# Kernel tuning notes

Hardware: AMD Instinct MI355X
Metric: run time of the kernel (lower is better)

## Reference

```python
import jax, jax.numpy as jnp
import numpy as np

TANH_CONST = 2.5
TEMPERATURE = 5.0


def setup_inputs() -> dict:
    key = jax.random.key(0)
    ks = jax.random.split(key, 9)
    B, L, NB, H, NC = 16384, 64, 8, 128, 1000
    return {
        "class_ids": jax.random.randint(ks[0], (B,), 0, NC),
        "gumbel_u": jax.random.uniform(ks[1], (L, B, NB), dtype=jnp.float32),
        "g_emb": jax.random.normal(ks[2], (NC, H), dtype=jnp.float32) * 0.1,
        "w_emb": jax.random.normal(ks[3], (NB, H), dtype=jnp.float32) * 0.1,
        "w_soft": jax.random.normal(ks[4], (NB, H), dtype=jnp.float32) * 0.1,
        "w_ih": jax.random.normal(ks[5], (4 * H, H), dtype=jnp.float32) * 0.1,
        "w_hh": jax.random.normal(ks[6], (4 * H, H), dtype=jnp.float32) * 0.1,
        "b_ih": jax.random.normal(ks[7], (4 * H,), dtype=jnp.float32) * 0.1,
        "b_hh": jax.random.normal(ks[8], (4 * H,), dtype=jnp.float32) * 0.1,
    }


def reference(class_ids, gumbel_u, g_emb, w_emb, w_soft, w_ih, w_hh, b_ih, b_hh):
    B = class_ids.shape[0]
    H = g_emb.shape[1]
    x0 = g_emb[class_ids]                      # [B, H] class embedding (reused each step)
    h0 = jnp.zeros((B, H), x0.dtype)
    c0 = jnp.zeros((B, H), x0.dtype)

    def step(carry, u):
        h, c, x = carry
        gates = x @ w_ih.T + h @ w_hh.T + b_ih + b_hh   # [B, 4H], torch gate order i,f,g,o
        i, f, g, o = jnp.split(gates, 4, axis=-1)
        c2 = jax.nn.sigmoid(f) * c + jax.nn.sigmoid(i) * jnp.tanh(g)
        h2 = jax.nn.sigmoid(o) * jnp.tanh(c2)
        logit = h2 @ w_soft.T                           # [B, NB]
        logit = TANH_CONST * jnp.tanh(logit / TEMPERATURE)
        # categorical sample via gumbel-max
        uc = jnp.clip(u, 1e-8, 1.0 - 1e-8)
        gmb = -jnp.log(-jnp.log(uc))
        branch = jnp.argmax(logit + gmb, axis=-1)       # [B] int
        logp = jax.nn.log_softmax(logit, axis=-1)
        lp = jnp.take_along_axis(logp, branch[:, None], axis=1)[:, 0]
        ent = -jnp.sum(jnp.exp(logp) * logp, axis=-1)
        x2 = (w_emb[branch] + x0) * 0.5
        return (h2, c2, x2), (branch, lp, ent)

    _, (arcs, lps, ents) = jax.lax.scan(step, (h0, c0, x0), gumbel_u)
    # stack along dim=1 like torch.stack(..., dim=1) -> [B, L]
    sample_arc = arcs.T
    sample_log_prob = lps.T
    sample_entropy = ents.T
    sample_prob = jnp.exp(sample_log_prob)
    return sample_arc, sample_log_prob, sample_entropy, sample_prob
```

## Files before the change

kernel.cpp:

```cpp
#include <hip/hip_runtime.h>
#include <math.h>

#define HD 128
#define NBR 8
#define LSTEPS 64
#define TILE_B 32
#define HT_PAD 36
#define PART_PAD 132

#define WPT_OFF   0
#define WIPT_OFF  65536
#define PP_OFF    131072
#define BSUM_OFF  135168

__global__ __launch_bounds__(256) void setup_kernel(
    const float* __restrict__ w_emb, const float* __restrict__ w_ih,
    const float* __restrict__ w_hh, const float* __restrict__ b_ih,
    const float* __restrict__ b_hh, float* __restrict__ ws)
{
  int tid = blockIdx.x * blockDim.x + threadIdx.x;
  if (tid < 65536) {
    int k = tid >> 9, col = tid & 511;
    int hh = col >> 2, q = col & 3;
    ws[WPT_OFF + tid]  = w_hh[(q*HD + hh)*HD + k];
    ws[WIPT_OFF + tid] = w_ih[(q*HD + hh)*HD + k];
  }
  if (tid < 4096) {
    int j = tid >> 9, rem = tid & 511;
    int q = rem >> 7, hh2 = rem & 127;
    const float* wr = w_ih + (q*HD + hh2)*HD;
    const float* er = w_emb + j*HD;
    float s = 0.f;
    for (int k = 0; k < HD; ++k) s = fmaf(er[k], wr[k], s);
    ws[PP_OFF + (size_t)j*512 + 4*hh2 + q] = s + b_ih[q*HD + hh2] + b_hh[q*HD + hh2];
  }
  if (tid < 512) {
    int q = tid >> 7, hh2 = tid & 127;
    ws[BSUM_OFF + tid] = b_ih[q*HD + hh2] + b_hh[q*HD + hh2];
  }
}

__device__ __forceinline__ float fsig(float x) {
  return __fdividef(1.f, 1.f + __expf(-x));
}
__device__ __forceinline__ float ftanh(float x) {
  float ax = fabsf(x);
  float e  = __expf(-2.f * ax);
  float r  = __fdividef(1.f - e, 1.f + e);
  return copysignf(r, x);
}

#define ROWQ(qi, wq, HA, HB) \
  acc[qi][0] = fmaf((HA).x, wq, acc[qi][0]); acc[qi][1] = fmaf((HA).y, wq, acc[qi][1]); \
  acc[qi][2] = fmaf((HA).z, wq, acc[qi][2]); acc[qi][3] = fmaf((HA).w, wq, acc[qi][3]); \
  acc[qi][4] = fmaf((HB).x, wq, acc[qi][4]); acc[qi][5] = fmaf((HB).y, wq, acc[qi][5]); \
  acc[qi][6] = fmaf((HB).z, wq, acc[qi][6]); acc[qi][7] = fmaf((HB).w, wq, acc[qi][7]);

#define KFMA(W, HA, HB) \
  ROWQ(0, (W).x, HA, HB) ROWQ(1, (W).y, HA, HB) ROWQ(2, (W).z, HA, HB) ROWQ(3, (W).w, HA, HB)

#define BAR_LGKM() asm volatile("s_waitcnt lgkmcnt(0)\n\ts_barrier" ::: "memory")

__global__ __launch_bounds__(512, 4) void ctrl_kernel(
    const int* __restrict__ class_ids,
    const float* __restrict__ gumbel_u,
    const float* __restrict__ g_emb,
    const float* __restrict__ w_soft,
    const float* __restrict__ ws,
    float* __restrict__ out,
    int Btot)
{
  __shared__ __align__(16) float hT0[HD * HT_PAD];
  __shared__ __align__(16) float hT1[HD * HT_PAD];
  __shared__ __align__(16) float wsoft_l[NBR * HD];
  __shared__ __align__(16) float part_l[TILE_B * PART_PAD];
  __shared__ __align__(16) float pp_l[NBR * 512];
  __shared__ int br_l[TILE_B];

  const int tid = threadIdx.x;
  const int b0  = blockIdx.x * TILE_B;
  const size_t BL = (size_t)Btot * LSTEPS;

  const float* __restrict__ wpT  = ws + WPT_OFF;
  const float* __restrict__ wipT = ws + WIPT_OFF;

  for (int i = tid; i < NBR*HD; i += 512) wsoft_l[i] = w_soft[i];
  for (int i = tid; i < NBR*512; i += 512) pp_l[i] = ws[PP_OFF + i];

  const int hh = tid & 127;
  const int bg = tid >> 7;
  const int slb = tid >> 4;
  const int sr  = tid & 15;

  {
    int sb = tid >> 4;
    int kc = tid & 15;
    int cid = class_ids[b0 + sb];
    const float* src = g_emb + (size_t)cid * HD + kc*8;
    float4 v0 = *(const float4*)(src);
    float4 v1 = *(const float4*)(src + 4);
    int kb = kc*8;
    hT0[(kb+0)*HT_PAD + sb] = v0.x;
    hT0[(kb+1)*HT_PAD + sb] = v0.y;
    hT0[(kb+2)*HT_PAD + sb] = v0.z;
    hT0[(kb+3)*HT_PAD + sb] = v0.w;
    hT0[(kb+4)*HT_PAD + sb] = v1.x;
    hT0[(kb+5)*HT_PAD + sb] = v1.y;
    hT0[(kb+6)*HT_PAD + sb] = v1.z;
    hT0[(kb+7)*HT_PAD + sb] = v1.w;
  }
  __syncthreads();

  float qpark[32];
  {
    float acc[4][8];
    #pragma unroll
    for (int q = 0; q < 4; ++q)
      #pragma unroll
      for (int j = 0; j < 8; ++j) acc[q][j] = 0.f;

    const float* wr = wipT + 4*hh;
    const float* hr = hT0 + bg*8;
    #pragma unroll 2
    for (int k = 0; k < HD; ++k) {
      float4 w  = *(const float4*)(wr);
      float4 ha = *(const float4*)(hr);
      float4 hb = *(const float4*)(hr + 4);
      KFMA(w, ha, hb);
      wr += 512; hr += HT_PAD;
    }
    #pragma unroll
    for (int q = 0; q < 4; ++q) {
      float bs = ws[BSUM_OFF + q*HD + hh];
      #pragma unroll
      for (int j = 0; j < 8; ++j) {
        float v = 0.5f * (acc[q][j] + bs);
        asm("v_accvgpr_write_b32 %0, %1" : "=a"(qpark[q*8+j]) : "v"(v));
      }
    }
  }
  __syncthreads();

  float c[8];
  #pragma unroll
  for (int j = 0; j < 8; ++j) c[j] = 0.f;

  float* hcur = hT0;
  float* hnxt = hT1;

  for (int t = 0; t < LSTEPS; ++t) {
    float gmb[8];
    if (sr == 0) {
      const float* up = gumbel_u + ((size_t)t * Btot + (b0 + slb)) * NBR;
      float4 ua = *(const float4*)up;
      float4 ub = *(const float4*)(up + 4);
      float uv[8] = {ua.x,ua.y,ua.z,ua.w,ub.x,ub.y,ub.z,ub.w};
      #pragma unroll
      for (int nb = 0; nb < 8; ++nb) {
        float uc = fminf(fmaxf(uv[nb], 1e-8f), 0.99999999f);
        gmb[nb] = -__logf(-__logf(uc));
      }
    }

    float acc[4][8];
    #pragma unroll
    for (int q = 0; q < 4; ++q)
      #pragma unroll
      for (int j = 0; j < 8; ++j)
        asm("v_accvgpr_read_b32 %0, %1" : "=v"(acc[q][j]) : "a"(qpark[q*8+j]));

    if (t > 0) {
      __builtin_amdgcn_s_setprio(1);
      const float* wr = wpT + 4*hh;
      const float* hr = hcur + bg*8;
      float4 w0 = *(const float4*)(wr);
      float4 w1 = *(const float4*)(wr + 512);
      float4 a0 = *(const float4*)(hr);
      float4 b0v = *(const float4*)(hr + 4);
      float4 a1 = *(const float4*)(hr + HT_PAD);
      float4 b1 = *(const float4*)(hr + HT_PAD + 4);
      #pragma unroll 3
      for (int kb = 0; kb < 63; ++kb) {
        float4 wc = w0, ac = a0, bc = b0v;
        w0  = *(const float4*)(wr + 2*512);
        a0  = *(const float4*)(hr + 2*HT_PAD);
        b0v = *(const float4*)(hr + 2*HT_PAD + 4);
        KFMA(wc, ac, bc);
        float4 wd = w1, ad = a1, bd = b1;
        w1 = *(const float4*)(wr + 3*512);
        a1 = *(const float4*)(hr + 3*HT_PAD);
        b1 = *(const float4*)(hr + 3*HT_PAD + 4);
        KFMA(wd, ad, bd);
        wr += 1024; hr += 2*HT_PAD;
      }
      KFMA(w0, a0, b0v);
      KFMA(w1, a1, b1);
      __builtin_amdgcn_s_setprio(0);
    }

    float h2v[8];
    #pragma unroll
    for (int j = 0; j < 8; ++j) {
      float gi, gf, gg, go;
      if (t == 0) {
        gi = 2.f*acc[0][j]; gf = 2.f*acc[1][j];
        gg = 2.f*acc[2][j]; go = 2.f*acc[3][j];
      } else {
        int br = br_l[bg*8 + j];
        float4 pv = *(const float4*)(&pp_l[br*512 + 4*hh]);
        gi = fmaf(0.5f, pv.x, acc[0][j]);
        gf = fmaf(0.5f, pv.y, acc[1][j]);
        gg = fmaf(0.5f, pv.z, acc[2][j]);
        go = fmaf(0.5f, pv.w, acc[3][j]);
      }
      float iv = fsig(gi);
      float fv = fsig(gf);
      float gv = ftanh(gg);
      float ov = fsig(go);
      float c2 = fmaf(fv, c[j], iv*gv);
      c[j] = c2;
      h2v[j] = ov * ftanh(c2);
    }

    {
      float* dst = &hnxt[hh*HT_PAD + bg*8];
      *(float4*)(dst)   = make_float4(h2v[0],h2v[1],h2v[2],h2v[3]);
      *(float4*)(dst+4) = make_float4(h2v[4],h2v[5],h2v[6],h2v[7]);
    }
    BAR_LGKM();

    {
      int lb = tid & 31, ch = tid >> 5;
      const float* hp = hnxt + (ch*8)*HT_PAD + lb;
      float hv[8];
      #pragma unroll
      for (int i = 0; i < 8; ++i) hv[i] = hp[i*HT_PAD];
      #pragma unroll
      for (int nb = 0; nb < 8; ++nb) {
        const float4* wr2 = (const float4*)&wsoft_l[nb*HD + ch*8];
        float4 wa = wr2[0], wb = wr2[1];
        float p = 0.f;
        p = fmaf(hv[0], wa.x, p); p = fmaf(hv[1], wa.y, p);
        p = fmaf(hv[2], wa.z, p); p = fmaf(hv[3], wa.w, p);
        p = fmaf(hv[4], wb.x, p); p = fmaf(hv[5], wb.y, p);
        p = fmaf(hv[6], wb.z, p); p = fmaf(hv[7], wb.w, p);
        part_l[lb*PART_PAD + nb*16 + ch] = p;
      }
    }
    BAR_LGKM();

    {
      float s[8];
      #pragma unroll
      for (int nb = 0; nb < 8; ++nb)
        s[nb] = part_l[slb*PART_PAD + nb*16 + sr];
      #pragma unroll
      for (int mk = 1; mk < 16; mk <<= 1) {
        #pragma unroll
        for (int nb = 0; nb < 8; ++nb)
          s[nb] += __shfl_xor(s[nb], mk, 64);
      }
      if (sr == 0) {
        float lg[8];
        #pragma unroll
        for (int nb = 0; nb < 8; ++nb)
          lg[nb] = 2.5f * ftanh(s[nb] * 0.2f);
        int br = 0; float best = lg[0] + gmb[0];
        #pragma unroll
        for (int nb = 1; nb < 8; ++nb) {
          float y = lg[nb] + gmb[nb];
          if (y > best) { best = y; br = nb; }
        }
        br_l[slb] = br;
        float m = lg[0];
        #pragma unroll
        for (int nb = 1; nb < 8; ++nb) m = fmaxf(m, lg[nb]);
        float se = 0.f;
        #pragma unroll
        for (int nb = 0; nb < 8; ++nb) se += __expf(lg[nb] - m);
        float lse = __logf(se);
        float lp = (lg[br] - m) - lse;
        float ent = 0.f;
        #pragma unroll
        for (int nb = 0; nb < 8; ++nb) {
          float lpi = (lg[nb] - m) - lse;
          ent -= __expf(lpi) * lpi;
        }
        size_t row = (size_t)(b0 + slb) * LSTEPS + t;
        out[row]        = (float)br;
        out[BL + row]   = lp;
        out[2*BL + row] = ent;
        out[3*BL + row] = __expf(lp);
      }
    }
    BAR_LGKM();

    float* tmp = hcur; hcur = hnxt; hnxt = tmp;
  }
}

extern "C" void kernel_launch(void* const* d_in, const int* in_sizes, int n_in,
                              void* d_out, int out_size, void* d_ws, size_t ws_size,
                              hipStream_t stream) {
  const int*   class_ids = (const int*)d_in[0];
  const float* gumbel_u  = (const float*)d_in[1];
  const float* g_emb     = (const float*)d_in[2];
  const float* w_emb     = (const float*)d_in[3];
  const float* w_soft    = (const float*)d_in[4];
  const float* w_ih      = (const float*)d_in[5];
  const float* w_hh      = (const float*)d_in[6];
  const float* b_ih      = (const float*)d_in[7];
  const float* b_hh      = (const float*)d_in[8];
  float* out = (float*)d_out;
  float* ws  = (float*)d_ws;
  int B = in_sizes[0];

  hipLaunchKernelGGL(setup_kernel, dim3(256), dim3(256), 0, stream,
                     w_emb, w_ih, w_hh, b_ih, b_hh, ws);
  hipLaunchKernelGGL(ctrl_kernel, dim3(B / TILE_B), dim3(512), 0, stream,
                     class_ids, gumbel_u, g_emb, w_soft, ws, out, B);
}
```

Baseline: 2.282 ms.

## Halve block threads and give each thread 16 batch columns per gate

Drops the recurrent LSTM kernel from 512 to 256 threads per block, so each thread now computes 4 gates × 16 batch rows instead of 4 × 8. Each loaded weight float4 is reused across twice as many batch rows, which cuts global/L2 weight traffic per FMA, and the logit reduction and scratch padding are resized to match. The cost is twice the register pressure for accumulators and parked AGPR values, and launch bounds drop to 256 threads × 2 blocks. That lowers occupancy and latency hiding, and the per-step serial work per thread doubles.

```diff
diff --git a/kernel.cpp b/kernel.cpp
--- a/kernel.cpp
+++ b/kernel.cpp
@@ -6,7 +6,7 @@
 #define LSTEPS 64
 #define TILE_B 32
 #define HT_PAD 36
-#define PART_PAD 132
+#define PART_PAD 68
 
 #define WPT_OFF   0
 #define WIPT_OFF  65536
@@ -50,18 +50,28 @@
   return copysignf(r, x);
 }
 
-#define ROWQ(qi, wq, HA, HB) \
-  acc[qi][0] = fmaf((HA).x, wq, acc[qi][0]); acc[qi][1] = fmaf((HA).y, wq, acc[qi][1]); \
-  acc[qi][2] = fmaf((HA).z, wq, acc[qi][2]); acc[qi][3] = fmaf((HA).w, wq, acc[qi][3]); \
-  acc[qi][4] = fmaf((HB).x, wq, acc[qi][4]); acc[qi][5] = fmaf((HB).y, wq, acc[qi][5]); \
-  acc[qi][6] = fmaf((HB).z, wq, acc[qi][6]); acc[qi][7] = fmaf((HB).w, wq, acc[qi][7]);
-
-#define KFMA(W, HA, HB) \
-  ROWQ(0, (W).x, HA, HB) ROWQ(1, (W).y, HA, HB) ROWQ(2, (W).z, HA, HB) ROWQ(3, (W).w, HA, HB)
+#define ROWQ16(qi, wq) \
+  acc[qi][0]  = fmaf(ha.x, wq, acc[qi][0]);  acc[qi][1]  = fmaf(ha.y, wq, acc[qi][1]);  \
+  acc[qi][2]  = fmaf(ha.z, wq, acc[qi][2]);  acc[qi][3]  = fmaf(ha.w, wq, acc[qi][3]);  \
+  acc[qi][4]  = fmaf(hb.x, wq, acc[qi][4]);  acc[qi][5]  = fmaf(hb.y, wq, acc[qi][5]);  \
+  acc[qi][6]  = fmaf(hb.z, wq, acc[qi][6]);  acc[qi][7]  = fmaf(hb.w, wq, acc[qi][7]);  \
+  acc[qi][8]  = fmaf(hc.x, wq, acc[qi][8]);  acc[qi][9]  = fmaf(hc.y, wq, acc[qi][9]);  \
+  acc[qi][10] = fmaf(hc.z, wq, acc[qi][10]); acc[qi][11] = fmaf(hc.w, wq, acc[qi][11]); \
+  acc[qi][12] = fmaf(hd.x, wq, acc[qi][12]); acc[qi][13] = fmaf(hd.y, wq, acc[qi][13]); \
+  acc[qi][14] = fmaf(hd.z, wq, acc[qi][14]); acc[qi][15] = fmaf(hd.w, wq, acc[qi][15]);
+
+#define KFMA16(W) \
+  ROWQ16(0, (W).x) ROWQ16(1, (W).y) ROWQ16(2, (W).z) ROWQ16(3, (W).w)
+
+#define LOADH(HP) \
+  float4 ha = *(const float4*)(HP); \
+  float4 hb = *(const float4*)((HP) + 4); \
+  float4 hc = *(const float4*)((HP) + 8); \
+  float4 hd = *(const float4*)((HP) + 12);
 
 #define BAR_LGKM() asm volatile("s_waitcnt lgkmcnt(0)\n\ts_barrier" ::: "memory")
 
-__global__ __launch_bounds__(512, 4) void ctrl_kernel(
+__global__ __launch_bounds__(256, 2) void ctrl_kernel(
     const int* __restrict__ class_ids,
     const float* __restrict__ gumbel_u,
     const float* __restrict__ g_emb,
@@ -84,66 +94,63 @@
   const float* __restrict__ wpT  = ws + WPT_OFF;
   const float* __restrict__ wipT = ws + WIPT_OFF;
 
-  for (int i = tid; i < NBR*HD; i += 512) wsoft_l[i] = w_soft[i];
-  for (int i = tid; i < NBR*512; i += 512) pp_l[i] = ws[PP_OFF + i];
+  for (int i = tid; i < NBR*HD; i += 256) wsoft_l[i] = w_soft[i];
+  for (int i = tid; i < NBR*512; i += 256) pp_l[i] = ws[PP_OFF + i];
 
   const int hh = tid & 127;
   const int bg = tid >> 7;
-  const int slb = tid >> 4;
-  const int sr  = tid & 15;
+  const int slb = tid >> 3;
+  const int sr  = tid & 7;
 
   {
-    int sb = tid >> 4;
-    int kc = tid & 15;
+    int sb = tid >> 3;
+    int kc = tid & 7;
     int cid = class_ids[b0 + sb];
-    const float* src = g_emb + (size_t)cid * HD + kc*8;
-    float4 v0 = *(const float4*)(src);
-    float4 v1 = *(const float4*)(src + 4);
-    int kb = kc*8;
-    hT0[(kb+0)*HT_PAD + sb] = v0.x;
-    hT0[(kb+1)*HT_PAD + sb] = v0.y;
-    hT0[(kb+2)*HT_PAD + sb] = v0.z;
-    hT0[(kb+3)*HT_PAD + sb] = v0.w;
-    hT0[(kb+4)*HT_PAD + sb] = v1.x;
-    hT0[(kb+5)*HT_PAD + sb] = v1.y;
-    hT0[(kb+6)*HT_PAD + sb] = v1.z;
-    hT0[(kb+7)*HT_PAD + sb] = v1.w;
+    const float* src = g_emb + (size_t)cid * HD + kc*16;
+    #pragma unroll
+    for (int ii = 0; ii < 4; ++ii) {
+      float4 v = *(const float4*)(src + 4*ii);
+      int kb = kc*16 + 4*ii;
+      hT0[(kb+0)*HT_PAD + sb] = v.x;
+      hT0[(kb+1)*HT_PAD + sb] = v.y;
+      hT0[(kb+2)*HT_PAD + sb] = v.z;
+      hT0[(kb+3)*HT_PAD + sb] = v.w;
+    }
   }
   __syncthreads();
 
-  float qpark[32];
+  float qpark[64];
   {
-    float acc[4][8];
+    float acc[4][16];
     #pragma unroll
     for (int q = 0; q < 4; ++q)
       #pragma unroll
-      for (int j = 0; j < 8; ++j) acc[q][j] = 0.f;
+      for (int j = 0; j < 16; ++j) acc[q][j] = 0.f;
 
     const float* wr = wipT + 4*hh;
-    const float* hr = hT0 + bg*8;
+    const float* hr = hT0 + bg*16;
     #pragma unroll 2
     for (int k = 0; k < HD; ++k) {
-      float4 w  = *(const float4*)(wr);
-      float4 ha = *(const float4*)(hr);
-      float4 hb = *(const float4*)(hr + 4);
-      KFMA(w, ha, hb);
+      float4 w = *(const float4*)(wr);
+      LOADH(hr);
+      KFMA16(w);
       wr += 512; hr += HT_PAD;
     }
     #pragma unroll
     for (int q = 0; q < 4; ++q) {
       float bs = ws[BSUM_OFF + q*HD + hh];
       #pragma unroll
-      for (int j = 0; j < 8; ++j) {
+      for (int j = 0; j < 16; ++j) {
         float v = 0.5f * (acc[q][j] + bs);
-        asm("v_accvgpr_write_b32 %0, %1" : "=a"(qpark[q*8+j]) : "v"(v));
+        asm("v_accvgpr_write_b32 %0, %1" : "=a"(qpark[q*16+j]) : "v"(v));
       }
     }
   }
   __syncthreads();
 
-  float c[8];
+  float c[16];
   #pragma unroll
-  for (int j = 0; j < 8; ++j) c[j] = 0.f;
+  for (int j = 0; j < 16; ++j) c[j] = 0.f;
 
   float* hcur = hT0;
   float* hnxt = hT1;
@@ -162,51 +169,49 @@
       }
     }
 
-    float acc[4][8];
+    float acc[4][16];
     #pragma unroll
     for (int q = 0; q < 4; ++q)
       #pragma unroll
-      for (int j = 0; j < 8; ++j)
-        asm("v_accvgpr_read_b32 %0, %1" : "=v"(acc[q][j]) : "a"(qpark[q*8+j]));
+      for (int j = 0; j < 16; ++j)
+        asm("v_accvgpr_read_b32 %0, %1" : "=v"(acc[q][j]) : "a"(qpark[q*16+j]));
 
     if (t > 0) {
       __builtin_amdgcn_s_setprio(1);
       const float* wr = wpT + 4*hh;
-      const float* hr = hcur + bg*8;
+      const float* hr = hcur + bg*16;
       float4 w0 = *(const float4*)(wr);
       float4 w1 = *(const float4*)(wr + 512);
-      float4 a0 = *(const float4*)(hr);
-      float4 b0v = *(const float4*)(hr + 4);
-      float4 a1 = *(const float4*)(hr + HT_PAD);
-      float4 b1 = *(const float4*)(hr + HT_PAD + 4);
-      #pragma unroll 3
+      #pragma unroll 2
       for (int kb = 0; kb < 63; ++kb) {
-        float4 wc = w0, ac = a0, bc = b0v;
-        w0  = *(const float4*)(wr + 2*512);
-        a0  = *(const float4*)(hr + 2*HT_PAD);
-        b0v = *(const float4*)(hr + 2*HT_PAD + 4);
-        KFMA(wc, ac, bc);
-        float4 wd = w1, ad = a1, bd = b1;
-        w1 = *(const float4*)(wr + 3*512);
-        a1 = *(const float4*)(hr + 3*HT_PAD);
-        b1 = *(const float4*)(hr + 3*HT_PAD + 4);
-        KFMA(wd, ad, bd);
+        {
+          float4 wc = w0;
+          w0 = *(const float4*)(wr + 2*512);
+          LOADH(hr);
+          KFMA16(wc);
+        }
+        {
+          float4 wc = w1;
+          w1 = *(const float4*)(wr + 3*512);
+          LOADH(hr + HT_PAD);
+          KFMA16(wc);
+        }
         wr += 1024; hr += 2*HT_PAD;
       }
-      KFMA(w0, a0, b0v);
-      KFMA(w1, a1, b1);
+      { LOADH(hr);          KFMA16(w0); }
+      { LOADH(hr + HT_PAD); KFMA16(w1); }
       __builtin_amdgcn_s_setprio(0);
     }
 
-    float h2v[8];
-    #pragma unroll
-    for (int j = 0; j < 8; ++j) {
+    float h2v[16];
+    #pragma unroll
+    for (int j = 0; j < 16; ++j) {
       float gi, gf, gg, go;
       if (t == 0) {
         gi = 2.f*acc[0][j]; gf = 2.f*acc[1][j];
         gg = 2.f*acc[2][j]; go = 2.f*acc[3][j];
       } else {
-        int br = br_l[bg*8 + j];
+        int br = br_l[bg*16 + j];
         float4 pv = *(const float4*)(&pp_l[br*512 + 4*hh]);
         gi = fmaf(0.5f, pv.x, acc[0][j]);
         gf = fmaf(0.5f, pv.y, acc[1][j]);
@@ -223,28 +228,34 @@
     }
 
     {
-      float* dst = &hnxt[hh*HT_PAD + bg*8];
-      *(float4*)(dst)   = make_float4(h2v[0],h2v[1],h2v[2],h2v[3]);
-      *(float4*)(dst+4) = make_float4(h2v[4],h2v[5],h2v[6],h2v[7]);
+      float* dst = &hnxt[hh*HT_PAD + bg*16];
+      *(float4*)(dst)    = make_float4(h2v[0], h2v[1], h2v[2], h2v[3]);
+      *(float4*)(dst+4)  = make_float4(h2v[4], h2v[5], h2v[6], h2v[7]);
+      *(float4*)(dst+8)  = make_float4(h2v[8], h2v[9], h2v[10],h2v[11]);
+      *(float4*)(dst+12) = make_float4(h2v[12],h2v[13],h2v[14],h2v[15]);
     }
     BAR_LGKM();
 
     {
       int lb = tid & 31, ch = tid >> 5;
-      const float* hp = hnxt + (ch*8)*HT_PAD + lb;
-      float hv[8];
-      #pragma unroll
-      for (int i = 0; i < 8; ++i) hv[i] = hp[i*HT_PAD];
+      const float* hp = hnxt + (ch*16)*HT_PAD + lb;
+      float hv[16];
+      #pragma unroll
+      for (int i = 0; i < 16; ++i) hv[i] = hp[i*HT_PAD];
       #pragma unroll
       for (int nb = 0; nb < 8; ++nb) {
-        const float4* wr2 = (const float4*)&wsoft_l[nb*HD + ch*8];
-        float4 wa = wr2[0], wb = wr2[1];
+        const float4* wr2 = (const float4*)&wsoft_l[nb*HD + ch*16];
+        float4 wa = wr2[0], wb = wr2[1], wc = wr2[2], wd = wr2[3];
         float p = 0.f;
-        p = fmaf(hv[0], wa.x, p); p = fmaf(hv[1], wa.y, p);
-        p = fmaf(hv[2], wa.z, p); p = fmaf(hv[3], wa.w, p);
-        p = fmaf(hv[4], wb.x, p); p = fmaf(hv[5], wb.y, p);
-        p = fmaf(hv[6], wb.z, p); p = fmaf(hv[7], wb.w, p);
-        part_l[lb*PART_PAD + nb*16 + ch] = p;
+        p = fmaf(hv[0],  wa.x, p); p = fmaf(hv[1],  wa.y, p);
+        p = fmaf(hv[2],  wa.z, p); p = fmaf(hv[3],  wa.w, p);
+        p = fmaf(hv[4],  wb.x, p); p = fmaf(hv[5],  wb.y, p);
+        p = fmaf(hv[6],  wb.z, p); p = fmaf(hv[7],  wb.w, p);
+        p = fmaf(hv[8],  wc.x, p); p = fmaf(hv[9],  wc.y, p);
+        p = fmaf(hv[10], wc.z, p); p = fmaf(hv[11], wc.w, p);
+        p = fmaf(hv[12], wd.x, p); p = fmaf(hv[13], wd.y, p);
+        p = fmaf(hv[14], wd.z, p); p = fmaf(hv[15], wd.w, p);
+        part_l[lb*PART_PAD + nb*8 + ch] = p;
       }
     }
     BAR_LGKM();
@@ -253,9 +264,9 @@
       float s[8];
       #pragma unroll
       for (int nb = 0; nb < 8; ++nb)
-        s[nb] = part_l[slb*PART_PAD + nb*16 + sr];
-      #pragma unroll
-      for (int mk = 1; mk < 16; mk <<= 1) {
+        s[nb] = part_l[slb*PART_PAD + nb*8 + sr];
+      #pragma unroll
+      for (int mk = 1; mk < 8; mk <<= 1) {
         #pragma unroll
         for (int nb = 0; nb < 8; ++nb)
           s[nb] += __shfl_xor(s[nb], mk, 64);
@@ -317,6 +328,6 @@
 
   hipLaunchKernelGGL(setup_kernel, dim3(256), dim3(256), 0, stream,
                      w_emb, w_ih, w_hh, b_ih, b_hh, ws);
-  hipLaunchKernelGGL(ctrl_kernel, dim3(B / TILE_B), dim3(512), 0, stream,
+  hipLaunchKernelGGL(ctrl_kernel, dim3(B / TILE_B), dim3(256), 0, stream,
                      class_ids, gumbel_u, g_emb, w_soft, ws, out, B);
 }
```

New measurement: 2.432 ms. 1.07x slower.

## Stage recurrent weights into LDS via async global_load_lds double buffering

Applied to the files above, without the earlier changes.

The recurrent h@W_hh matmul now streams W_hh in 16 KB chunks into a double-buffered LDS staging area with global_load_lds, instead of each thread reading float4 weights straight from global/L2. The branch-projection table pp is staged into the same buffer at the end, and the two h buffers collapse into one, which frees LDS. This trades direct per-thread global loads for 16 extra block-wide barriers per step plus vmcnt waits. The goal is to cut redundant L2 traffic across the 4 batch-groups that share weights and to reduce LDS footprint.

```diff
diff --git a/kernel.cpp b/kernel.cpp
--- a/kernel.cpp
+++ b/kernel.cpp
@@ -50,6 +50,12 @@
   return copysignf(r, x);
 }
 
+__device__ __forceinline__ void gload16(const float* g, float* l) {
+  __builtin_amdgcn_global_load_lds(
+      (const __attribute__((address_space(1))) void*)(g),
+      (__attribute__((address_space(3))) void*)(l), 16, 0, 0);
+}
+
 #define ROWQ(qi, wq, HA, HB) \
   acc[qi][0] = fmaf((HA).x, wq, acc[qi][0]); acc[qi][1] = fmaf((HA).y, wq, acc[qi][1]); \
   acc[qi][2] = fmaf((HA).z, wq, acc[qi][2]); acc[qi][3] = fmaf((HA).w, wq, acc[qi][3]); \
@@ -59,7 +65,22 @@
 #define KFMA(W, HA, HB) \
   ROWQ(0, (W).x, HA, HB) ROWQ(1, (W).y, HA, HB) ROWQ(2, (W).z, HA, HB) ROWQ(3, (W).w, HA, HB)
 
+#define CONSUME(WB, HR) do { \
+    _Pragma("unroll") \
+    for (int kk = 0; kk < 8; ++kk) { \
+      float4 w  = *(const float4*)((WB) + kk*512 + (hh << 2)); \
+      float4 ha = *(const float4*)((HR) + kk*HT_PAD); \
+      float4 hb = *(const float4*)((HR) + kk*HT_PAD + 4); \
+      KFMA(w, ha, hb); \
+    } } while (0)
+
+#define STAGE16K(GSRC, LBUF) do { \
+    gload16((GSRC) + t4,        (LBUF) + wb4); \
+    gload16((GSRC) + 2048 + t4, (LBUF) + 2048 + wb4); \
+  } while (0)
+
 #define BAR_LGKM() asm volatile("s_waitcnt lgkmcnt(0)\n\ts_barrier" ::: "memory")
+#define BAR_FULL() asm volatile("s_waitcnt vmcnt(0) lgkmcnt(0)\n\ts_barrier" ::: "memory")
 
 __global__ __launch_bounds__(512, 4) void ctrl_kernel(
     const int* __restrict__ class_ids,
@@ -70,11 +91,10 @@
     float* __restrict__ out,
     int Btot)
 {
-  __shared__ __align__(16) float hT0[HD * HT_PAD];
-  __shared__ __align__(16) float hT1[HD * HT_PAD];
+  __shared__ __align__(16) float hT[HD * HT_PAD];
   __shared__ __align__(16) float wsoft_l[NBR * HD];
   __shared__ __align__(16) float part_l[TILE_B * PART_PAD];
-  __shared__ __align__(16) float pp_l[NBR * 512];
+  __shared__ __align__(16) float wstage[2 * 4096];
   __shared__ int br_l[TILE_B];
 
   const int tid = threadIdx.x;
@@ -83,14 +103,16 @@
 
   const float* __restrict__ wpT  = ws + WPT_OFF;
   const float* __restrict__ wipT = ws + WIPT_OFF;
+  const float* __restrict__ ppg  = ws + PP_OFF;
 
   for (int i = tid; i < NBR*HD; i += 512) wsoft_l[i] = w_soft[i];
-  for (int i = tid; i < NBR*512; i += 512) pp_l[i] = ws[PP_OFF + i];
 
   const int hh = tid & 127;
   const int bg = tid >> 7;
   const int slb = tid >> 4;
   const int sr  = tid & 15;
+  const int t4  = tid << 2;
+  const int wb4 = __builtin_amdgcn_readfirstlane((tid & 448) << 2);
 
   {
     int sb = tid >> 4;
@@ -100,14 +122,14 @@
     float4 v0 = *(const float4*)(src);
     float4 v1 = *(const float4*)(src + 4);
     int kb = kc*8;
-    hT0[(kb+0)*HT_PAD + sb] = v0.x;
-    hT0[(kb+1)*HT_PAD + sb] = v0.y;
-    hT0[(kb+2)*HT_PAD + sb] = v0.z;
-    hT0[(kb+3)*HT_PAD + sb] = v0.w;
-    hT0[(kb+4)*HT_PAD + sb] = v1.x;
-    hT0[(kb+5)*HT_PAD + sb] = v1.y;
-    hT0[(kb+6)*HT_PAD + sb] = v1.z;
-    hT0[(kb+7)*HT_PAD + sb] = v1.w;
+    hT[(kb+0)*HT_PAD + sb] = v0.x;
+    hT[(kb+1)*HT_PAD + sb] = v0.y;
+    hT[(kb+2)*HT_PAD + sb] = v0.z;
+    hT[(kb+3)*HT_PAD + sb] = v0.w;
+    hT[(kb+4)*HT_PAD + sb] = v1.x;
+    hT[(kb+5)*HT_PAD + sb] = v1.y;
+    hT[(kb+6)*HT_PAD + sb] = v1.z;
+    hT[(kb+7)*HT_PAD + sb] = v1.w;
   }
   __syncthreads();
 
@@ -120,7 +142,7 @@
       for (int j = 0; j < 8; ++j) acc[q][j] = 0.f;
 
     const float* wr = wipT + 4*hh;
-    const float* hr = hT0 + bg*8;
+    const float* hr = hT + bg*8;
     #pragma unroll 2
     for (int k = 0; k < HD; ++k) {
       float4 w  = *(const float4*)(wr);
@@ -145,9 +167,6 @@
   #pragma unroll
   for (int j = 0; j < 8; ++j) c[j] = 0.f;
 
-  float* hcur = hT0;
-  float* hnxt = hT1;
-
   for (int t = 0; t < LSTEPS; ++t) {
     float gmb[8];
     if (sr == 0) {
@@ -171,30 +190,17 @@
 
     if (t > 0) {
       __builtin_amdgcn_s_setprio(1);
-      const float* wr = wpT + 4*hh;
-      const float* hr = hcur + bg*8;
-      float4 w0 = *(const float4*)(wr);
-      float4 w1 = *(const float4*)(wr + 512);
-      float4 a0 = *(const float4*)(hr);
-      float4 b0v = *(const float4*)(hr + 4);
-      float4 a1 = *(const float4*)(hr + HT_PAD);
-      float4 b1 = *(const float4*)(hr + HT_PAD + 4);
-      #pragma unroll 3
-      for (int kb = 0; kb < 63; ++kb) {
-        float4 wc = w0, ac = a0, bc = b0v;
-        w0  = *(const float4*)(wr + 2*512);
-        a0  = *(const float4*)(hr + 2*HT_PAD);
-        b0v = *(const float4*)(hr + 2*HT_PAD + 4);
-        KFMA(wc, ac, bc);
-        float4 wd = w1, ad = a1, bd = b1;
-        w1 = *(const float4*)(wr + 3*512);
-        a1 = *(const float4*)(hr + 3*HT_PAD);
-        b1 = *(const float4*)(hr + 3*HT_PAD + 4);
-        KFMA(wd, ad, bd);
-        wr += 1024; hr += 2*HT_PAD;
-      }
-      KFMA(w0, a0, b0v);
-      KFMA(w1, a1, b1);
+      const float* hrb = hT + bg*8;
+      #pragma unroll 1
+      for (int cc = 0; cc < 8; ++cc) {
+        STAGE16K(wpT + (2*cc+1)*4096, wstage + 4096);
+        CONSUME(wstage, hrb + (2*cc*8)*HT_PAD);
+        BAR_FULL();
+        if (cc < 7) { STAGE16K(wpT + (2*cc+2)*4096, wstage); }
+        else        { STAGE16K(ppg, wstage); }
+        CONSUME(wstage + 4096, hrb + ((2*cc+1)*8)*HT_PAD);
+        BAR_FULL();
+      }
       __builtin_amdgcn_s_setprio(0);
     }
 
@@ -207,7 +213,7 @@
         gg = 2.f*acc[2][j]; go = 2.f*acc[3][j];
       } else {
         int br = br_l[bg*8 + j];
-        float4 pv = *(const float4*)(&pp_l[br*512 + 4*hh]);
+        float4 pv = *(const float4*)(&wstage[br*512 + 4*hh]);
         gi = fmaf(0.5f, pv.x, acc[0][j]);
         gf = fmaf(0.5f, pv.y, acc[1][j]);
         gg = fmaf(0.5f, pv.z, acc[2][j]);
@@ -223,15 +229,16 @@
     }
 
     {
-      float* dst = &hnxt[hh*HT_PAD + bg*8];
+      float* dst = &hT[hh*HT_PAD + bg*8];
       *(float4*)(dst)   = make_float4(h2v[0],h2v[1],h2v[2],h2v[3]);
       *(float4*)(dst+4) = make_float4(h2v[4],h2v[5],h2v[6],h2v[7]);
     }
     BAR_LGKM();
 
+    STAGE16K(wpT, wstage);
     {
       int lb = tid & 31, ch = tid >> 5;
-      const float* hp = hnxt + (ch*8)*HT_PAD + lb;
+      const float* hp = hT + (ch*8)*HT_PAD + lb;
       float hv[8];
       #pragma unroll
       for (int i = 0; i < 8; ++i) hv[i] = hp[i*HT_PAD];
@@ -293,9 +300,7 @@
         out[3*BL + row] = __expf(lp);
       }
     }
-    BAR_LGKM();
-
-    float* tmp = hcur; hcur = hnxt; hnxt = tmp;
+    BAR_FULL();
   }
 }
 
```

New measurement: 3.755 ms. 1.65x slower.
